# Optimization experiments

Measured on AMD Instinct MI355X. Metric: run time of the kernel, lower is better.

Reference implementation:

```python
import jax, jax.numpy as jnp
import numpy as np

N, D, L, K = 32, 128, 3136, 64

def setup_inputs() -> dict:
    key = jax.random.key(0)
    k1, k2, k3 = jax.random.split(key, 3)
    x = jax.random.normal(k1, (N, D, L), dtype=jnp.float32)
    weight = jax.random.normal(k2, (K, D), dtype=jnp.float32)  # codebook centers
    scale = jax.random.normal(k3, (1,), dtype=jnp.float32)
    return {"x": x, "weight": weight, "scale": scale}

def reference(x, weight, scale):
    # x: (N, C, ...) -> (N, D, L); output scaled squared L2 dist (N, K, L)
    n, c = x.shape[0], x.shape[1]
    xf = x.reshape(n, c, -1)  # (N, D, L)
    x_sq = jnp.sum(xf * xf, axis=1)          # (N, L)
    c_sq = jnp.sum(weight * weight, axis=1)  # (K,)
    xc = jnp.einsum('ndl,kd->nkl', xf, weight)  # (N, K, L)
    dist = x_sq[:, None, :] + c_sq[None, :, None] - 2.0 * xc
    return dist / (scale[0] ** 2)
```

## Files before the change

kernel.cpp:

```cpp
#include <hip/hip_runtime.h>

#define N_ 32
#define D_ 128
#define L_ 3136
#define K_ 64
#define WSTR 136

typedef short bf16x8 __attribute__((ext_vector_type(8)));
typedef float f32x4  __attribute__((ext_vector_type(4)));

__device__ inline unsigned short f2bf(float f) {
    unsigned u = __float_as_uint(f);
    return (unsigned short)((u + 0x7FFFu + ((u >> 16) & 1u)) >> 16);
}
__device__ inline float bf2f(unsigned short h) {
    return __uint_as_float(((unsigned)h) << 16);
}

__global__ __launch_bounds__(256, 4) void enc_mfma_kernel(
    const float* __restrict__ x,
    const float* __restrict__ w,
    const float* __restrict__ scale,
    float* __restrict__ out)
{
    __shared__ __attribute__((aligned(16))) unsigned short lds_wl[K_ * WSTR];
    __shared__ __attribute__((aligned(16))) char lds_u[K_ * WSTR * 2];
    __shared__ float lds_csqp[4][64];
    __shared__ float lds_csq[K_];
    __shared__ float lds_xsq[64];

    unsigned short* lds_wh = (unsigned short*)lds_u;
    float* lds_c = (float*)lds_u;

    const int t    = threadIdx.x;
    const int wave = t >> 6;
    const int lane = t & 63;
    const int col  = lane & 15;
    const int quad = lane >> 4;

    const int n  = blockIdx.y;
    const int l0 = blockIdx.x * 64;

    {
        const int k = t & 63, q = t >> 6;
        const float* wr = w + (size_t)k * D_ + q * 32;
        float s = 0.f;
        for (int j = 0; j < 32; j += 4) {
            float4 v = *(const float4*)(wr + j);
            float vv[4] = {v.x, v.y, v.z, v.w};
            __attribute__((aligned(8))) unsigned short hbuf[4], lbuf[4];
#pragma unroll
            for (int c = 0; c < 4; ++c) {
                s = fmaf(vv[c], vv[c], s);
                unsigned short h = f2bf(vv[c]);
                hbuf[c] = h;
                lbuf[c] = f2bf(vv[c] - bf2f(h));
            }
            const int off = k * WSTR + q * 32 + j;
            *(ushort4*)&lds_wh[off] = *(const ushort4*)hbuf;
            *(ushort4*)&lds_wl[off] = *(const ushort4*)lbuf;
        }
        lds_csqp[q][k] = s;
    }
    __syncthreads();
    if (t < K_)
        lds_csq[t] = lds_csqp[0][t] + lds_csqp[1][t] + lds_csqp[2][t] + lds_csqp[3][t];

    const float* xa = x + (size_t)n * D_ * L_ + l0 + wave * 16 + col;

    f32x4 acc[4];
#pragma unroll
    for (int kt = 0; kt < 4; ++kt) acc[kt] = (f32x4){0.f, 0.f, 0.f, 0.f};
    float xsq = 0.f;

#pragma unroll
    for (int dc = 0; dc < 4; ++dc) {
        const float* xp = xa + (size_t)(dc * 32 + quad * 8) * L_;
        float xv[8];
#pragma unroll
        for (int j = 0; j < 8; ++j) xv[j] = xp[(size_t)j * L_];

        __attribute__((aligned(16))) unsigned short ah[8], al[8];
#pragma unroll
        for (int j = 0; j < 8; ++j) {
            xsq = fmaf(xv[j], xv[j], xsq);
            unsigned short h = f2bf(xv[j]);
            ah[j] = h;
            al[j] = f2bf(xv[j] - bf2f(h));
        }
        bf16x8 afh = *(const bf16x8*)ah;
        bf16x8 afl = *(const bf16x8*)al;

        const int wb = dc * 32 + quad * 8;
#pragma unroll
        for (int kt = 0; kt < 4; ++kt) {
            const int row = kt * 16 + col;
            bf16x8 bh = *(const bf16x8*)&lds_wh[row * WSTR + wb];
            bf16x8 bl = *(const bf16x8*)&lds_wl[row * WSTR + wb];
            acc[kt] = __builtin_amdgcn_mfma_f32_16x16x32_bf16(afh, bh, acc[kt], 0, 0, 0);
            acc[kt] = __builtin_amdgcn_mfma_f32_16x16x32_bf16(afl, bh, acc[kt], 0, 0, 0);
            acc[kt] = __builtin_amdgcn_mfma_f32_16x16x32_bf16(afh, bl, acc[kt], 0, 0, 0);
        }
    }

    xsq += __shfl_xor(xsq, 16, 64);
    xsq += __shfl_xor(xsq, 32, 64);
    if (quad == 0) lds_xsq[wave * 16 + col] = xsq;

    __syncthreads();

#pragma unroll
    for (int kt = 0; kt < 4; ++kt) {
        const int kk = kt * 16 + col;
#pragma unroll
        for (int r = 0; r < 4; ++r) {
            const int ll = wave * 16 + quad * 4 + r;
            lds_c[kk * 65 + ll] = acc[kt][r];
        }
    }
    __syncthreads();

    const float sc = scale[0];
    const float inv_s2 = 1.0f / (sc * sc);
    float* op = out + (size_t)n * K_ * L_ + l0;
#pragma unroll
    for (int it = 0; it < 16; ++it) {
        const int idx = it * 256 + t;
        const int kk = idx >> 6, ll = idx & 63;
        op[(size_t)kk * L_ + ll] =
            (lds_xsq[ll] + lds_csq[kk] - 2.0f * lds_c[kk * 65 + ll]) * inv_s2;
    }
}

extern "C" void kernel_launch(void* const* d_in, const int* in_sizes, int n_in,
                              void* d_out, int out_size, void* d_ws, size_t ws_size,
                              hipStream_t stream) {
    const float* x     = (const float*)d_in[0];
    const float* w     = (const float*)d_in[1];
    const float* scale = (const float*)d_in[2];
    float* out = (float*)d_out;

    dim3 grid(L_ / 64, N_);
    enc_mfma_kernel<<<grid, 256, 0, stream>>>(x, w, scale, out);
}
```

Before: 100.8 us.

## Process two batch items per block to amortize codebook staging

Each block now handles two batch samples for the same L tile, so the per-block conversion of the codebook into split-bf16 LDS planes and its norm computation are shared across twice the work. The grid halves along N, and per-thread register use roughly doubles for accumulators and inputs. The LDS result buffers are reorganized to hold both outputs by reusing the two weight planes. In exchange there are fewer blocks (784) and higher register pressure, which may reduce occupancy below the launch-bounds target.

```diff
diff --git a/kernel.cpp b/kernel.cpp
--- a/kernel.cpp
+++ b/kernel.cpp
@@ -5,6 +5,7 @@
 #define L_ 3136
 #define K_ 64
 #define WSTR 136
+#define WPLANE (K_ * WSTR * 2)
 
 typedef short bf16x8 __attribute__((ext_vector_type(8)));
 typedef float f32x4  __attribute__((ext_vector_type(4)));
@@ -23,14 +24,15 @@
     const float* __restrict__ scale,
     float* __restrict__ out)
 {
-    __shared__ __attribute__((aligned(16))) unsigned short lds_wl[K_ * WSTR];
-    __shared__ __attribute__((aligned(16))) char lds_u[K_ * WSTR * 2];
+    __shared__ __attribute__((aligned(16))) char lds_u[WPLANE * 2];
     __shared__ float lds_csqp[4][64];
     __shared__ float lds_csq[K_];
-    __shared__ float lds_xsq[64];
+    __shared__ float lds_xsq[2][64];
 
     unsigned short* lds_wh = (unsigned short*)lds_u;
-    float* lds_c = (float*)lds_u;
+    unsigned short* lds_wl = (unsigned short*)(lds_u + WPLANE);
+    float* lds_c0 = (float*)lds_u;
+    float* lds_c1 = (float*)(lds_u + WPLANE);
 
     const int t    = threadIdx.x;
     const int wave = t >> 6;
@@ -38,7 +40,7 @@
     const int col  = lane & 15;
     const int quad = lane >> 4;
 
-    const int n  = blockIdx.y;
+    const int n0 = blockIdx.y * 2;
     const int l0 = blockIdx.x * 64;
 
     {
@@ -66,30 +68,42 @@
     if (t < K_)
         lds_csq[t] = lds_csqp[0][t] + lds_csqp[1][t] + lds_csqp[2][t] + lds_csqp[3][t];
 
-    const float* xa = x + (size_t)n * D_ * L_ + l0 + wave * 16 + col;
+    const float* xa0 = x + (size_t)n0 * D_ * L_ + l0 + wave * 16 + col;
+    const float* xa1 = xa0 + (size_t)D_ * L_;
 
-    f32x4 acc[4];
+    f32x4 acc0[4], acc1[4];
 #pragma unroll
-    for (int kt = 0; kt < 4; ++kt) acc[kt] = (f32x4){0.f, 0.f, 0.f, 0.f};
-    float xsq = 0.f;
+    for (int kt = 0; kt < 4; ++kt) {
+        acc0[kt] = (f32x4){0.f, 0.f, 0.f, 0.f};
+        acc1[kt] = (f32x4){0.f, 0.f, 0.f, 0.f};
+    }
+    float xsq0 = 0.f, xsq1 = 0.f;
 
 #pragma unroll
     for (int dc = 0; dc < 4; ++dc) {
-        const float* xp = xa + (size_t)(dc * 32 + quad * 8) * L_;
-        float xv[8];
+        const size_t doff = (size_t)(dc * 32 + quad * 8) * L_;
+        float xv0[8], xv1[8];
 #pragma unroll
-        for (int j = 0; j < 8; ++j) xv[j] = xp[(size_t)j * L_];
+        for (int j = 0; j < 8; ++j) xv0[j] = xa0[doff + (size_t)j * L_];
+#pragma unroll
+        for (int j = 0; j < 8; ++j) xv1[j] = xa1[doff + (size_t)j * L_];
 
-        __attribute__((aligned(16))) unsigned short ah[8], al[8];
+        __attribute__((aligned(16))) unsigned short ah0[8], al0[8], ah1[8], al1[8];
 #pragma unroll
         for (int j = 0; j < 8; ++j) {
-            xsq = fmaf(xv[j], xv[j], xsq);
-            unsigned short h = f2bf(xv[j]);
-            ah[j] = h;
-            al[j] = f2bf(xv[j] - bf2f(h));
+            xsq0 = fmaf(xv0[j], xv0[j], xsq0);
+            unsigned short h0 = f2bf(xv0[j]);
+            ah0[j] = h0;
+            al0[j] = f2bf(xv0[j] - bf2f(h0));
+            xsq1 = fmaf(xv1[j], xv1[j], xsq1);
+            unsigned short h1 = f2bf(xv1[j]);
+            ah1[j] = h1;
+            al1[j] = f2bf(xv1[j] - bf2f(h1));
         }
-        bf16x8 afh = *(const bf16x8*)ah;
-        bf16x8 afl = *(const bf16x8*)al;
+        bf16x8 afh0 = *(const bf16x8*)ah0;
+        bf16x8 afl0 = *(const bf16x8*)al0;
+        bf16x8 afh1 = *(const bf16x8*)ah1;
+        bf16x8 afl1 = *(const bf16x8*)al1;
 
         const int wb = dc * 32 + quad * 8;
 #pragma unroll
@@ -97,15 +111,23 @@
             const int row = kt * 16 + col;
             bf16x8 bh = *(const bf16x8*)&lds_wh[row * WSTR + wb];
             bf16x8 bl = *(const bf16x8*)&lds_wl[row * WSTR + wb];
-            acc[kt] = __builtin_amdgcn_mfma_f32_16x16x32_bf16(afh, bh, acc[kt], 0, 0, 0);
-            acc[kt] = __builtin_amdgcn_mfma_f32_16x16x32_bf16(afl, bh, acc[kt], 0, 0, 0);
-            acc[kt] = __builtin_amdgcn_mfma_f32_16x16x32_bf16(afh, bl, acc[kt], 0, 0, 0);
+            acc0[kt] = __builtin_amdgcn_mfma_f32_16x16x32_bf16(afh0, bh, acc0[kt], 0, 0, 0);
+            acc0[kt] = __builtin_amdgcn_mfma_f32_16x16x32_bf16(afl0, bh, acc0[kt], 0, 0, 0);
+            acc0[kt] = __builtin_amdgcn_mfma_f32_16x16x32_bf16(afh0, bl, acc0[kt], 0, 0, 0);
+            acc1[kt] = __builtin_amdgcn_mfma_f32_16x16x32_bf16(afh1, bh, acc1[kt], 0, 0, 0);
+            acc1[kt] = __builtin_amdgcn_mfma_f32_16x16x32_bf16(afl1, bh, acc1[kt], 0, 0, 0);
+            acc1[kt] = __builtin_amdgcn_mfma_f32_16x16x32_bf16(afh1, bl, acc1[kt], 0, 0, 0);
         }
     }
 
-    xsq += __shfl_xor(xsq, 16, 64);
-    xsq += __shfl_xor(xsq, 32, 64);
-    if (quad == 0) lds_xsq[wave * 16 + col] = xsq;
+    xsq0 += __shfl_xor(xsq0, 16, 64);
+    xsq0 += __shfl_xor(xsq0, 32, 64);
+    xsq1 += __shfl_xor(xsq1, 16, 64);
+    xsq1 += __shfl_xor(xsq1, 32, 64);
+    if (quad == 0) {
+        lds_xsq[0][wave * 16 + col] = xsq0;
+        lds_xsq[1][wave * 16 + col] = xsq1;
+    }
 
     __syncthreads();
 
@@ -115,20 +137,25 @@
 #pragma unroll
         for (int r = 0; r < 4; ++r) {
             const int ll = wave * 16 + quad * 4 + r;
-            lds_c[kk * 65 + ll] = acc[kt][r];
+            lds_c0[kk * 65 + ll] = acc0[kt][r];
+            lds_c1[kk * 65 + ll] = acc1[kt][r];
         }
     }
     __syncthreads();
 
     const float sc = scale[0];
     const float inv_s2 = 1.0f / (sc * sc);
-    float* op = out + (size_t)n * K_ * L_ + l0;
 #pragma unroll
-    for (int it = 0; it < 16; ++it) {
-        const int idx = it * 256 + t;
-        const int kk = idx >> 6, ll = idx & 63;
-        op[(size_t)kk * L_ + ll] =
-            (lds_xsq[ll] + lds_csq[kk] - 2.0f * lds_c[kk * 65 + ll]) * inv_s2;
+    for (int nn = 0; nn < 2; ++nn) {
+        const float* lc = nn ? lds_c1 : lds_c0;
+        float* op = out + (size_t)(n0 + nn) * K_ * L_ + l0;
+#pragma unroll
+        for (int it = 0; it < 16; ++it) {
+            const int idx = it * 256 + t;
+            const int kk = idx >> 6, ll = idx & 63;
+            op[(size_t)kk * L_ + ll] =
+                (lds_xsq[nn][ll] + lds_csq[kk] - 2.0f * lc[kk * 65 + ll]) * inv_s2;
+        }
     }
 }
 
@@ -140,6 +167,6 @@
     const float* scale = (const float*)d_in[2];
     float* out = (float*)d_out;
 
-    dim3 grid(L_ / 64, N_);
+    dim3 grid(L_ / 64, N_ / 2);
     enc_mfma_kernel<<<grid, 256, 0, stream>>>(x, w, scale, out);
 }
```

Result: no change. 101.6 us (+0.8%).

## Precompute split-bf16 codebook in prep kernel and DMA fragments into LDS

Applied to the files above, without the earlier changes.

Adds a small prep kernel that converts the codebook once into hi/lo bf16 fragments, already laid out in MFMA B-operand order, and computes the center norms into workspace. The main kernel then copies these fragments straight into LDS with global_load_lds instead of having every one of 1568 blocks redo the conversion and norm reduction. This removes the per-block prologue ALU work and one barrier. The cost is an extra kernel launch and a dependency between the two kernels. LDS reads of B become contiguous per-lane 16-byte loads.

```diff
diff --git a/kernel.cpp b/kernel.cpp
--- a/kernel.cpp
+++ b/kernel.cpp
@@ -4,7 +4,6 @@
 #define D_ 128
 #define L_ 3136
 #define K_ 64
-#define WSTR 136
 
 typedef short bf16x8 __attribute__((ext_vector_type(8)));
 typedef float f32x4  __attribute__((ext_vector_type(4)));
@@ -17,54 +16,81 @@
     return __uint_as_float(((unsigned)h) << 16);
 }
 
+__global__ __launch_bounds__(64) void prep_kernel(
+    const float* __restrict__ w,
+    unsigned short* __restrict__ whi,
+    unsigned short* __restrict__ wlo,
+    float* __restrict__ csq)
+{
+    const int b = blockIdx.x, lane = threadIdx.x;
+    if (b < 16) {
+        const int dc = b >> 2, kt = b & 3;
+        const int row = kt * 16 + (lane & 15);
+        const int d0  = dc * 32 + (lane >> 4) * 8;
+        const float* src = w + row * D_ + d0;
+        __attribute__((aligned(16))) unsigned short h[8], l[8];
+#pragma unroll
+        for (int j = 0; j < 8; ++j) {
+            float v = src[j];
+            h[j] = f2bf(v);
+            l[j] = f2bf(v - bf2f(h[j]));
+        }
+        const size_t off = (size_t)(b * 64 + lane) * 8;
+        *(ushort4*)(whi + off)     = *(const ushort4*)(h);
+        *(ushort4*)(whi + off + 4) = *(const ushort4*)(h + 4);
+        *(ushort4*)(wlo + off)     = *(const ushort4*)(l);
+        *(ushort4*)(wlo + off + 4) = *(const ushort4*)(l + 4);
+    } else {
+        const float* wr = w + lane * D_;
+        float s = 0.f;
+#pragma unroll
+        for (int d = 0; d < D_; d += 4) {
+            float4 v = *(const float4*)(wr + d);
+            s = fmaf(v.x, v.x, s); s = fmaf(v.y, v.y, s);
+            s = fmaf(v.z, v.z, s); s = fmaf(v.w, v.w, s);
+        }
+        csq[lane] = s;
+    }
+}
+
 __global__ __launch_bounds__(256, 4) void enc_mfma_kernel(
     const float* __restrict__ x,
-    const float* __restrict__ w,
+    const unsigned short* __restrict__ whi,
+    const unsigned short* __restrict__ wlo,
+    const float* __restrict__ csqg,
     const float* __restrict__ scale,
     float* __restrict__ out)
 {
-    __shared__ __attribute__((aligned(16))) unsigned short lds_wl[K_ * WSTR];
-    __shared__ __attribute__((aligned(16))) char lds_u[K_ * WSTR * 2];
-    __shared__ float lds_csqp[4][64];
+    __shared__ __attribute__((aligned(16))) unsigned short lds_w[2 * 8192];
     __shared__ float lds_csq[K_];
     __shared__ float lds_xsq[64];
-
-    unsigned short* lds_wh = (unsigned short*)lds_u;
-    float* lds_c = (float*)lds_u;
+    float* lds_c = (float*)lds_w;
 
     const int t    = threadIdx.x;
     const int wave = t >> 6;
     const int lane = t & 63;
     const int col  = lane & 15;
     const int quad = lane >> 4;
+    const int n    = blockIdx.y;
+    const int l0   = blockIdx.x * 64;
 
-    const int n  = blockIdx.y;
-    const int l0 = blockIdx.x * 64;
-
-    {
-        const int k = t & 63, q = t >> 6;
-        const float* wr = w + (size_t)k * D_ + q * 32;
-        float s = 0.f;
-        for (int j = 0; j < 32; j += 4) {
-            float4 v = *(const float4*)(wr + j);
-            float vv[4] = {v.x, v.y, v.z, v.w};
-            __attribute__((aligned(8))) unsigned short hbuf[4], lbuf[4];
 #pragma unroll
-            for (int c = 0; c < 4; ++c) {
-                s = fmaf(vv[c], vv[c], s);
-                unsigned short h = f2bf(vv[c]);
-                hbuf[c] = h;
-                lbuf[c] = f2bf(vv[c] - bf2f(h));
-            }
-            const int off = k * WSTR + q * 32 + j;
-            *(ushort4*)&lds_wh[off] = *(const ushort4*)hbuf;
-            *(ushort4*)&lds_wl[off] = *(const ushort4*)lbuf;
-        }
-        lds_csqp[q][k] = s;
+    for (int i = 0; i < 8; ++i) {
+        const int c = wave * 8 + i;
+        const unsigned short* g =
+            (c < 16 ? whi + (size_t)c * 512 : wlo + (size_t)(c - 16) * 512) + lane * 8;
+        __builtin_amdgcn_global_load_lds(
+            (const __attribute__((address_space(1))) unsigned int*)g,
+            (__attribute__((address_space(3))) unsigned int*)&lds_w[c * 512],
+            16, 0, 0);
+    }
+    if (wave == 0) {
+        __builtin_amdgcn_global_load_lds(
+            (const __attribute__((address_space(1))) unsigned int*)(csqg + lane),
+            (__attribute__((address_space(3))) unsigned int*)lds_csq,
+            4, 0, 0);
     }
     __syncthreads();
-    if (t < K_)
-        lds_csq[t] = lds_csqp[0][t] + lds_csqp[1][t] + lds_csqp[2][t] + lds_csqp[3][t];
 
     const float* xa = x + (size_t)n * D_ * L_ + l0 + wave * 16 + col;
 
@@ -91,12 +117,11 @@
         bf16x8 afh = *(const bf16x8*)ah;
         bf16x8 afl = *(const bf16x8*)al;
 
-        const int wb = dc * 32 + quad * 8;
 #pragma unroll
         for (int kt = 0; kt < 4; ++kt) {
-            const int row = kt * 16 + col;
-            bf16x8 bh = *(const bf16x8*)&lds_wh[row * WSTR + wb];
-            bf16x8 bl = *(const bf16x8*)&lds_wl[row * WSTR + wb];
+            const int fo = ((dc * 4 + kt) * 64 + lane) * 8;
+            bf16x8 bh = *(const bf16x8*)&lds_w[fo];
+            bf16x8 bl = *(const bf16x8*)&lds_w[8192 + fo];
             acc[kt] = __builtin_amdgcn_mfma_f32_16x16x32_bf16(afh, bh, acc[kt], 0, 0, 0);
             acc[kt] = __builtin_amdgcn_mfma_f32_16x16x32_bf16(afl, bh, acc[kt], 0, 0, 0);
             acc[kt] = __builtin_amdgcn_mfma_f32_16x16x32_bf16(afh, bl, acc[kt], 0, 0, 0);
@@ -140,6 +165,11 @@
     const float* scale = (const float*)d_in[2];
     float* out = (float*)d_out;
 
+    unsigned short* whi = (unsigned short*)d_ws;
+    unsigned short* wlo = (unsigned short*)((char*)d_ws + 16384);
+    float*          csq = (float*)((char*)d_ws + 32768);
+
+    prep_kernel<<<17, 64, 0, stream>>>(w, whi, wlo, csq);
     dim3 grid(L_ / 64, N_);
-    enc_mfma_kernel<<<grid, 256, 0, stream>>>(x, w, scale, out);
+    enc_mfma_kernel<<<grid, 256, 0, stream>>>(x, whi, wlo, csq, scale, out);
 }
```

Result: no change. 101.0 us (+0.1%).
